# Kernel tuning notes

Measured on AMD Instinct MI355X. Metric: run time of the kernel, lower is better.

Reference implementation:

```python
import jax, jax.numpy as jnp
import numpy as np

N = 100000
E = 1600000

def _gcn_layer(x, row, col, W, b):
    # gather neighbor feats then scatter-add into destination rows
    agg = jax.ops.segment_sum(x[col], row, num_segments=N)  # [N, d]
    deg = jax.ops.segment_sum(jnp.ones((row.shape[0],), x.dtype), row, num_segments=N)
    deg = jnp.clip(deg, 1.0, None)[:, None]  # [N, 1]
    return (agg / deg + x) @ W + b

def setup_inputs() -> dict:
    key = jax.random.key(0)
    ks = jax.random.split(key, 6)
    x = jax.random.normal(ks[0], (N, 64), dtype=jnp.float32)
    edge_index = jax.random.randint(ks[1], (2, E), 0, N, dtype=jnp.int64)
    W1 = jax.random.normal(ks[2], (64, 128), dtype=jnp.float32) * 0.1
    b1 = jax.random.normal(ks[3], (128,), dtype=jnp.float32) * 0.1
    W2 = jax.random.normal(ks[4], (128, 64), dtype=jnp.float32) * 0.1
    b2 = jax.random.normal(ks[5], (64,), dtype=jnp.float32) * 0.1
    return {"x": x, "edge_index": edge_index, "W1": W1, "b1": b1, "W2": W2, "b2": b2}

def reference(x, edge_index, W1, b1, W2, b2):
    row, col = edge_index[0], edge_index[1]
    h = jax.nn.relu(_gcn_layer(x, row, col, W1, b1))
    h = _gcn_layer(h, row, col, W2, b2)
    return h
```

## Files before the change

kernel.cpp:

```cpp
#include <hip/hip_runtime.h>
#include <stdint.h>

#define WS_ALIGN(x) (((x) + 255) & ~(size_t)255)
#define CSR_CAP 64
#define RPB 512
#define CAPB 9216

typedef __attribute__((ext_vector_type(8))) unsigned short ushort8_t;
typedef __attribute__((ext_vector_type(8))) short short8_t;
typedef __attribute__((ext_vector_type(4))) float float4_t;

static __device__ __forceinline__ unsigned short f2bf(float f) {
    unsigned u = __float_as_uint(f);
    unsigned r = (u + 0x7FFFu + ((u >> 16) & 1u)) >> 16;
    return (unsigned short)r;
}
static __device__ __forceinline__ float bf2f(unsigned short s) {
    return __uint_as_float(((unsigned)s) << 16);
}

__global__ void detect_idx_kernel(const int* __restrict__ p, int* __restrict__ flagOr) {
    int t = threadIdx.x;
    int v = 0;
    for (int i = t; i < 2048; i += 256) v |= p[2 * i + 1];
    if (v) atomicOr(flagOr, v);
}

__global__ void init_cursor_kernel(int* __restrict__ gCursor, int nb) {
    int i = blockIdx.x * 256 + threadIdx.x;
    if (i < nb) gCursor[i] = i * CAPB;
}

__global__ __launch_bounds__(256) void bucket_kernel(
    const void* __restrict__ eidx, int E, const int* __restrict__ flagOr,
    int nb, int* __restrict__ gCursor, int2* __restrict__ staging) {
    __shared__ int cnt[256];
    __shared__ int base[256];
    int t = threadIdx.x;
    if (t < nb) cnt[t] = 0;
    __syncthreads();

    int e0 = (blockIdx.x * 256 + t) * 8;
    bool is64 = (*flagOr == 0);
    int m = E - e0; if (m > 8) m = 8; if (m < 0) m = 0;
    int r[8], bk[8], slot[8];
    for (int j = 0; j < m; ++j) {
        r[j] = is64 ? (int)((const long long*)eidx)[e0 + j]
                    : ((const int*)eidx)[e0 + j];
        bk[j] = r[j] >> 9;
        slot[j] = atomicAdd(&cnt[bk[j]], 1);
    }
    __syncthreads();
    if (t < nb) base[t] = atomicAdd(&gCursor[t], cnt[t]);
    __syncthreads();
    for (int j = 0; j < m; ++j) {
        int c = is64 ? (int)((const long long*)eidx)[E + e0 + j]
                     : ((const int*)eidx)[E + e0 + j];
        int dst = base[bk[j]] + slot[j];
        if (dst < (bk[j] + 1) * CAPB) staging[dst] = make_int2(r[j], c);
    }
}

__global__ __launch_bounds__(1024) void ell_kernel(
    const int2* __restrict__ staging, const int* __restrict__ gCursor,
    int* __restrict__ csr, int* __restrict__ deg, int N) {
    __shared__ int lcnt[RPB];
    int b = blockIdx.x, t = threadIdx.x;
    if (t < RPB) lcnt[t] = 0;
    __syncthreads();
    int start = b * CAPB;
    int end = gCursor[b];
    if (end > start + CAPB) end = start + CAPB;
    for (int i = start + t; i < end; i += 1024) {
        int2 rc = staging[i];
        int lr = rc.x - (b << 9);
        int slot = atomicAdd(&lcnt[lr], 1);
        if (slot < CSR_CAP) csr[(size_t)rc.x * CSR_CAP + slot] = rc.y;
    }
    __syncthreads();
    int r = (b << 9) + t;
    if (t < RPB && r < N) deg[r] = lcnt[t];
}

__global__ void xcast_kernel(const float4* __restrict__ x, ushort4* __restrict__ xb,
                             int n4) {
    int i = blockIdx.x * 256 + threadIdx.x;
    if (i >= n4) return;
    float4 f = x[i];
    ushort4 o;
    o.x = f2bf(f.x); o.y = f2bf(f.y); o.z = f2bf(f.z); o.w = f2bf(f.w);
    xb[i] = o;
}

__global__ __launch_bounds__(256) void agg_kernel(
    const unsigned short* __restrict__ xb, const int* __restrict__ deg,
    const int* __restrict__ csr, unsigned short* __restrict__ v, int N) {
    int tid = threadIdx.x;
    int w = tid >> 6, lane = tid & 63;
    int oct = lane >> 3, fo = lane & 7;
    int n = blockIdx.x * 4 + w;
    if (n >= N) return;
    int d = deg[n];
    if (d > CSR_CAP) d = CSR_CAP;
    const int* row = &csr[(size_t)n * CSR_CAP];

    float a0 = 0, a1 = 0, a2 = 0, a3 = 0, a4 = 0, a5 = 0, a6 = 0, a7 = 0;
    int nIter = (d + 7) >> 3;
    int it = 0;
    for (; it + 2 <= nIter; it += 2) {
        int k0 = it * 8 + oct, k1 = k0 + 8;
        int i0 = (k0 < d) ? row[k0] : N;
        int i1 = (k1 < d) ? row[k1] : N;
        ushort8_t f0 = *(const ushort8_t*)&xb[(size_t)i0 * 64 + fo * 8];
        ushort8_t f1 = *(const ushort8_t*)&xb[(size_t)i1 * 64 + fo * 8];
        a0 += bf2f(f0[0]) + bf2f(f1[0]); a1 += bf2f(f0[1]) + bf2f(f1[1]);
        a2 += bf2f(f0[2]) + bf2f(f1[2]); a3 += bf2f(f0[3]) + bf2f(f1[3]);
        a4 += bf2f(f0[4]) + bf2f(f1[4]); a5 += bf2f(f0[5]) + bf2f(f1[5]);
        a6 += bf2f(f0[6]) + bf2f(f1[6]); a7 += bf2f(f0[7]) + bf2f(f1[7]);
    }
    if (it < nIter) {
        int k0 = it * 8 + oct;
        int i0 = (k0 < d) ? row[k0] : N;
        ushort8_t f0 = *(const ushort8_t*)&xb[(size_t)i0 * 64 + fo * 8];
        a0 += bf2f(f0[0]); a1 += bf2f(f0[1]); a2 += bf2f(f0[2]); a3 += bf2f(f0[3]);
        a4 += bf2f(f0[4]); a5 += bf2f(f0[5]); a6 += bf2f(f0[6]); a7 += bf2f(f0[7]);
    }
    #define RED(m) a0 += __shfl_xor(a0, m); a1 += __shfl_xor(a1, m); \
                   a2 += __shfl_xor(a2, m); a3 += __shfl_xor(a3, m); \
                   a4 += __shfl_xor(a4, m); a5 += __shfl_xor(a5, m); \
                   a6 += __shfl_xor(a6, m); a7 += __shfl_xor(a7, m);
    RED(8) RED(16) RED(32)
    #undef RED

    if (oct == 0) {
        ushort8_t s = *(const ushort8_t*)&xb[(size_t)n * 64 + fo * 8];
        float inv = 1.0f / (float)(d > 1 ? d : 1);
        ushort8_t o;
        o[0] = f2bf(a0 * inv + bf2f(s[0])); o[1] = f2bf(a1 * inv + bf2f(s[1]));
        o[2] = f2bf(a2 * inv + bf2f(s[2])); o[3] = f2bf(a3 * inv + bf2f(s[3]));
        o[4] = f2bf(a4 * inv + bf2f(s[4])); o[5] = f2bf(a5 * inv + bf2f(s[5]));
        o[6] = f2bf(a6 * inv + bf2f(s[6])); o[7] = f2bf(a7 * inv + bf2f(s[7]));
        *(ushort8_t*)&v[(size_t)n * 64 + fo * 8] = o;
    }
}

__global__ __launch_bounds__(256) void mlp_kernel(
    const unsigned short* __restrict__ v, const float* __restrict__ W1,
    const float* __restrict__ b1, const float* __restrict__ W2,
    unsigned short* __restrict__ g16, int N) {
    __shared__ unsigned short vA[64 * 72];
    __shared__ unsigned short W1t[128 * 72];
    __shared__ unsigned short hA[64 * 136];
    __shared__ unsigned short W2t[64 * 136];
    int t = threadIdx.x;
    int node0 = blockIdx.x * 64;

    for (int i = t; i < 1024; i += 256) {
        int node = i >> 4, k0 = (i & 15) * 4;
        int gn = node0 + node;
        ushort4 val = make_ushort4(0, 0, 0, 0);
        if (gn < N) val = *(const ushort4*)&v[(size_t)gn * 64 + k0];
        *(ushort4*)&vA[node * 72 + k0] = val;
    }
    for (int i = t; i < 8192; i += 256) {
        int k = i >> 7, col = i & 127;
        W1t[col * 72 + k] = f2bf(W1[i]);
    }
    for (int i = t; i < 8192; i += 256) {
        int k = i >> 6, col = i & 63;
        W2t[col * 136 + k] = f2bf(W2[i]);
    }
    __syncthreads();

    int w = t >> 6, lane = t & 63;
    int l15 = lane & 15, quad = lane >> 4;
    const float4_t fzero = {0.f, 0.f, 0.f, 0.f};

    short8_t af[4][2];
    #pragma unroll
    for (int ms = 0; ms < 4; ++ms)
        #pragma unroll
        for (int kk = 0; kk < 2; ++kk)
            af[ms][kk] = *(const short8_t*)&vA[(ms * 16 + l15) * 72 + kk * 32 + quad * 8];
    short8_t bf1[2][2];
    #pragma unroll
    for (int cs = 0; cs < 2; ++cs)
        #pragma unroll
        for (int kk = 0; kk < 2; ++kk)
            bf1[cs][kk] = *(const short8_t*)&W1t[((w * 2 + cs) * 16 + l15) * 72 + kk * 32 + quad * 8];

    float4_t acc1[4][2];
    #pragma unroll
    for (int ms = 0; ms < 4; ++ms)
        #pragma unroll
        for (int cs = 0; cs < 2; ++cs)
            acc1[ms][cs] = fzero;
    #pragma unroll
    for (int ms = 0; ms < 4; ++ms)
        #pragma unroll
        for (int cs = 0; cs < 2; ++cs) {
            acc1[ms][cs] = __builtin_amdgcn_mfma_f32_16x16x32_bf16(af[ms][0], bf1[cs][0], acc1[ms][cs], 0, 0, 0);
            acc1[ms][cs] = __builtin_amdgcn_mfma_f32_16x16x32_bf16(af[ms][1], bf1[cs][1], acc1[ms][cs], 0, 0, 0);
        }

    #pragma unroll
    for (int cs = 0; cs < 2; ++cs) {
        int col = (w * 2 + cs) * 16 + l15;
        float bias = b1[col];
        #pragma unroll
        for (int ms = 0; ms < 4; ++ms) {
            #pragma unroll
            for (int r = 0; r < 4; ++r) {
                int node = ms * 16 + quad * 4 + r;
                hA[node * 136 + col] = f2bf(fmaxf(acc1[ms][cs][r] + bias, 0.f));
            }
        }
    }
    __syncthreads();

    short8_t bh[4];
    #pragma unroll
    for (int kk = 0; kk < 4; ++kk)
        bh[kk] = *(const short8_t*)&W2t[(w * 16 + l15) * 136 + kk * 32 + quad * 8];

    #pragma unroll
    for (int ms = 0; ms < 4; ++ms) {
        float4_t acc2 = fzero;
        #pragma unroll
        for (int kk = 0; kk < 4; ++kk) {
            short8_t ah = *(const short8_t*)&hA[(ms * 16 + l15) * 136 + kk * 32 + quad * 8];
            acc2 = __builtin_amdgcn_mfma_f32_16x16x32_bf16(ah, bh[kk], acc2, 0, 0, 0);
        }
        #pragma unroll
        for (int r = 0; r < 4; ++r) {
            int gn = node0 + ms * 16 + quad * 4 + r;
            if (gn < N) g16[(size_t)gn * 64 + w * 16 + l15] = f2bf(acc2[r]);
        }
    }
}

__global__ __launch_bounds__(256) void final_kernel(
    const unsigned short* __restrict__ g16, const float* __restrict__ b2,
    const int* __restrict__ deg, const int* __restrict__ csr,
    float* __restrict__ out, int N) {
    int tid = threadIdx.x;
    int w = tid >> 6, lane = tid & 63;
    int oct = lane >> 3, fo = lane & 7;
    int n = blockIdx.x * 4 + w;
    if (n >= N) return;
    int d = deg[n];
    if (d > CSR_CAP) d = CSR_CAP;
    const int* row = &csr[(size_t)n * CSR_CAP];

    float a0 = 0, a1 = 0, a2 = 0, a3 = 0, a4 = 0, a5 = 0, a6 = 0, a7 = 0;
    int nIter = (d + 7) >> 3;
    int it = 0;
    for (; it + 2 <= nIter; it += 2) {
        int k0 = it * 8 + oct, k1 = k0 + 8;
        int i0 = (k0 < d) ? row[k0] : N;
        int i1 = (k1 < d) ? row[k1] : N;
        ushort8_t f0 = *(const ushort8_t*)&g16[(size_t)i0 * 64 + fo * 8];
        ushort8_t f1 = *(const ushort8_t*)&g16[(size_t)i1 * 64 + fo * 8];
        a0 += bf2f(f0[0]) + bf2f(f1[0]); a1 += bf2f(f0[1]) + bf2f(f1[1]);
        a2 += bf2f(f0[2]) + bf2f(f1[2]); a3 += bf2f(f0[3]) + bf2f(f1[3]);
        a4 += bf2f(f0[4]) + bf2f(f1[4]); a5 += bf2f(f0[5]) + bf2f(f1[5]);
        a6 += bf2f(f0[6]) + bf2f(f1[6]); a7 += bf2f(f0[7]) + bf2f(f1[7]);
    }
    if (it < nIter) {
        int k0 = it * 8 + oct;
        int i0 = (k0 < d) ? row[k0] : N;
        ushort8_t f0 = *(const ushort8_t*)&g16[(size_t)i0 * 64 + fo * 8];
        a0 += bf2f(f0[0]); a1 += bf2f(f0[1]); a2 += bf2f(f0[2]); a3 += bf2f(f0[3]);
        a4 += bf2f(f0[4]); a5 += bf2f(f0[5]); a6 += bf2f(f0[6]); a7 += bf2f(f0[7]);
    }
    #define RED(m) a0 += __shfl_xor(a0, m); a1 += __shfl_xor(a1, m); \
                   a2 += __shfl_xor(a2, m); a3 += __shfl_xor(a3, m); \
                   a4 += __shfl_xor(a4, m); a5 += __shfl_xor(a5, m); \
                   a6 += __shfl_xor(a6, m); a7 += __shfl_xor(a7, m);
    RED(8) RED(16) RED(32)
    #undef RED

    if (oct == 0) {
        ushort8_t s = *(const ushort8_t*)&g16[(size_t)n * 64 + fo * 8];
        float4 bzA = ((const float4*)b2)[fo * 2];
        float4 bzB = ((const float4*)b2)[fo * 2 + 1];
        float inv = 1.0f / (float)(d > 1 ? d : 1);
        float4 oA, oB;
        oA.x = a0 * inv + bf2f(s[0]) + bzA.x;
        oA.y = a1 * inv + bf2f(s[1]) + bzA.y;
        oA.z = a2 * inv + bf2f(s[2]) + bzA.z;
        oA.w = a3 * inv + bf2f(s[3]) + bzA.w;
        oB.x = a4 * inv + bf2f(s[4]) + bzB.x;
        oB.y = a5 * inv + bf2f(s[5]) + bzB.y;
        oB.z = a6 * inv + bf2f(s[6]) + bzB.z;
        oB.w = a7 * inv + bf2f(s[7]) + bzB.w;
        *(float4*)&out[(size_t)n * 64 + fo * 8] = oA;
        *(float4*)&out[(size_t)n * 64 + fo * 8 + 4] = oB;
    }
}

extern "C" void kernel_launch(void* const* d_in, const int* in_sizes, int n_in,
                              void* d_out, int out_size, void* d_ws, size_t ws_size,
                              hipStream_t stream) {
    const float* x  = (const float*)d_in[0];
    const void*  ei = d_in[1];
    const float* W1 = (const float*)d_in[2];
    const float* b1 = (const float*)d_in[3];
    const float* W2 = (const float*)d_in[4];
    const float* b2 = (const float*)d_in[5];
    float* out = (float*)d_out;

    int N = out_size / 64;
    int E = in_sizes[1] / 2;
    int nb = (N + RPB - 1) / RPB;

    char* ws = (char*)d_ws;
    size_t off = 0;
    auto alloc = [&](size_t bytes) { size_t r = off; off += WS_ALIGN(bytes); return r; };
    int* flagOr  = (int*)(ws + alloc(4));
    int* gCursor = (int*)(ws + alloc((size_t)4 * nb));
    int* deg     = (int*)(ws + alloc((size_t)4 * N));
    int* csr     = (int*)(ws + alloc((size_t)4 * N * CSR_CAP));
    char* bufA   = ws + alloc((size_t)128 * (N + 1));
    unsigned short* xb  = (unsigned short*)bufA;
    unsigned short* g16 = (unsigned short*)bufA;
    unsigned short* v   = (unsigned short*)(ws + alloc((size_t)128 * N));
    int2* staging = (int2*)(ws + alloc((size_t)8 * nb * CAPB));
    (void)ws_size;

    hipMemsetAsync(flagOr, 0, 4, stream);
    hipMemsetAsync(bufA + (size_t)128 * N, 0, 128, stream);

    detect_idx_kernel<<<1, 256, 0, stream>>>((const int*)ei, flagOr);
    init_cursor_kernel<<<(nb + 255) / 256, 256, 0, stream>>>(gCursor, nb);

    int b1blocks = (E + 2047) / 2048;
    bucket_kernel<<<b1blocks, 256, 0, stream>>>(ei, E, flagOr, nb, gCursor, staging);
    ell_kernel<<<nb, 1024, 0, stream>>>(staging, gCursor, csr, deg, N);

    xcast_kernel<<<(N * 16 + 255) / 256, 256, 0, stream>>>((const float4*)x, (ushort4*)xb, N * 16);
    agg_kernel<<<(N + 3) / 4, 256, 0, stream>>>(xb, deg, csr, v, N);
    mlp_kernel<<<(N + 63) / 64, 256, 0, stream>>>(v, W1, b1, W2, g16, N);
    final_kernel<<<(N + 3) / 4, 256, 0, stream>>>(g16, b2, deg, csr, out, N);
}
```

Measured before the change: 250.6 us.

## Fuse prep kernels, fuse aggregation into MLP, pack staging entries, change gather mapping

Merges the bf16 cast, index-width detection, cursor init, sentinel zeroing and one-time weight transposition into a single prep kernel, so weights are no longer transposed in every MLP block. Fuses the first-layer aggregation into the MLP kernel so aggregated rows go straight to shared memory instead of a global buffer. Packs staging entries into 32-bit words (local row plus column), which halves bucket traffic. Remaps the gather so each half-wave handles one node with 4-byte loads over 4 neighbours at a time, with no shuffle reduction. Risks: the packing limits column indices to 17 bits, and the fused kernel has less parallelism per block during the gather phase.

```diff
diff --git a/kernel.cpp b/kernel.cpp
--- a/kernel.cpp
+++ b/kernel.cpp
@@ -6,7 +6,6 @@
 #define RPB 512
 #define CAPB 9216
 
-typedef __attribute__((ext_vector_type(8))) unsigned short ushort8_t;
 typedef __attribute__((ext_vector_type(8))) short short8_t;
 typedef __attribute__((ext_vector_type(4))) float float4_t;
 
@@ -19,21 +18,48 @@
     return __uint_as_float(((unsigned)s) << 16);
 }
 
-__global__ void detect_idx_kernel(const int* __restrict__ p, int* __restrict__ flagOr) {
-    int t = threadIdx.x;
-    int v = 0;
-    for (int i = t; i < 2048; i += 256) v |= p[2 * i + 1];
-    if (v) atomicOr(flagOr, v);
-}
-
-__global__ void init_cursor_kernel(int* __restrict__ gCursor, int nb) {
-    int i = blockIdx.x * 256 + threadIdx.x;
-    if (i < nb) gCursor[i] = i * CAPB;
+__global__ __launch_bounds__(256) void prep_kernel(
+    const float4* __restrict__ x, ushort4* __restrict__ xb, int n4,
+    const int* __restrict__ eip, int* __restrict__ flagOr,
+    const float* __restrict__ W1, unsigned short* __restrict__ W1t,
+    const float* __restrict__ W2, unsigned short* __restrict__ W2t,
+    int* __restrict__ gCursor, int nb,
+    unsigned short* __restrict__ sentX, unsigned short* __restrict__ sentG) {
+    int gt = blockIdx.x * 256 + threadIdx.x;
+    if (gt < n4) {
+        float4 f = x[gt];
+        ushort4 o;
+        o.x = f2bf(f.x); o.y = f2bf(f.y); o.z = f2bf(f.z); o.w = f2bf(f.w);
+        xb[gt] = o;
+        return;
+    }
+    int r = gt - n4;
+    if (r < 8192) {
+        int k = r >> 7, col = r & 127;
+        W1t[col * 64 + k] = f2bf(W1[r]);
+        return;
+    }
+    r -= 8192;
+    if (r < 8192) {
+        int k = r >> 6, col = r & 63;
+        W2t[col * 128 + k] = f2bf(W2[r]);
+        return;
+    }
+    r -= 8192;
+    if (r < 256) { if (r < nb) gCursor[r] = r * CAPB; return; }
+    r -= 256;
+    if (r < 64) { sentX[r] = 0; sentG[r] = 0; return; }
+    r -= 64;
+    if (r < 256) {
+        int v = 0;
+        for (int i = r; i < 2048; i += 256) v |= eip[2 * i + 1];
+        if (v) atomicOr(flagOr, v);
+    }
 }
 
 __global__ __launch_bounds__(256) void bucket_kernel(
     const void* __restrict__ eidx, int E, const int* __restrict__ flagOr,
-    int nb, int* __restrict__ gCursor, int2* __restrict__ staging) {
+    int nb, int* __restrict__ gCursor, unsigned* __restrict__ staging) {
     __shared__ int cnt[256];
     __shared__ int base[256];
     int t = threadIdx.x;
@@ -57,12 +83,13 @@
         int c = is64 ? (int)((const long long*)eidx)[E + e0 + j]
                      : ((const int*)eidx)[E + e0 + j];
         int dst = base[bk[j]] + slot[j];
-        if (dst < (bk[j] + 1) * CAPB) staging[dst] = make_int2(r[j], c);
+        if (dst < (bk[j] + 1) * CAPB)
+            staging[dst] = ((unsigned)(r[j] & (RPB - 1)) << 17) | (unsigned)c;
     }
 }
 
 __global__ __launch_bounds__(1024) void ell_kernel(
-    const int2* __restrict__ staging, const int* __restrict__ gCursor,
+    const unsigned* __restrict__ staging, const int* __restrict__ gCursor,
     int* __restrict__ csr, int* __restrict__ deg, int N) {
     __shared__ int lcnt[RPB];
     int b = blockIdx.x, t = threadIdx.x;
@@ -72,122 +99,75 @@
     int end = gCursor[b];
     if (end > start + CAPB) end = start + CAPB;
     for (int i = start + t; i < end; i += 1024) {
-        int2 rc = staging[i];
-        int lr = rc.x - (b << 9);
+        unsigned u = staging[i];
+        int lr = (int)(u >> 17);
+        int c  = (int)(u & 0x1FFFF);
         int slot = atomicAdd(&lcnt[lr], 1);
-        if (slot < CSR_CAP) csr[(size_t)rc.x * CSR_CAP + slot] = rc.y;
-    }
-    __syncthreads();
-    int r = (b << 9) + t;
-    if (t < RPB && r < N) deg[r] = lcnt[t];
-}
-
-__global__ void xcast_kernel(const float4* __restrict__ x, ushort4* __restrict__ xb,
-                             int n4) {
-    int i = blockIdx.x * 256 + threadIdx.x;
-    if (i >= n4) return;
-    float4 f = x[i];
-    ushort4 o;
-    o.x = f2bf(f.x); o.y = f2bf(f.y); o.z = f2bf(f.z); o.w = f2bf(f.w);
-    xb[i] = o;
-}
-
-__global__ __launch_bounds__(256) void agg_kernel(
+        if (slot < CSR_CAP) csr[(size_t)((b << 9) + lr) * CSR_CAP + slot] = c;
+    }
+    __syncthreads();
+    int rr = (b << 9) + t;
+    if (t < RPB && rr < N) deg[rr] = lcnt[t];
+}
+
+__global__ __launch_bounds__(256) void agg_mlp_kernel(
     const unsigned short* __restrict__ xb, const int* __restrict__ deg,
-    const int* __restrict__ csr, unsigned short* __restrict__ v, int N) {
-    int tid = threadIdx.x;
-    int w = tid >> 6, lane = tid & 63;
-    int oct = lane >> 3, fo = lane & 7;
-    int n = blockIdx.x * 4 + w;
-    if (n >= N) return;
-    int d = deg[n];
-    if (d > CSR_CAP) d = CSR_CAP;
-    const int* row = &csr[(size_t)n * CSR_CAP];
-
-    float a0 = 0, a1 = 0, a2 = 0, a3 = 0, a4 = 0, a5 = 0, a6 = 0, a7 = 0;
-    int nIter = (d + 7) >> 3;
-    int it = 0;
-    for (; it + 2 <= nIter; it += 2) {
-        int k0 = it * 8 + oct, k1 = k0 + 8;
-        int i0 = (k0 < d) ? row[k0] : N;
-        int i1 = (k1 < d) ? row[k1] : N;
-        ushort8_t f0 = *(const ushort8_t*)&xb[(size_t)i0 * 64 + fo * 8];
-        ushort8_t f1 = *(const ushort8_t*)&xb[(size_t)i1 * 64 + fo * 8];
-        a0 += bf2f(f0[0]) + bf2f(f1[0]); a1 += bf2f(f0[1]) + bf2f(f1[1]);
-        a2 += bf2f(f0[2]) + bf2f(f1[2]); a3 += bf2f(f0[3]) + bf2f(f1[3]);
-        a4 += bf2f(f0[4]) + bf2f(f1[4]); a5 += bf2f(f0[5]) + bf2f(f1[5]);
-        a6 += bf2f(f0[6]) + bf2f(f1[6]); a7 += bf2f(f0[7]) + bf2f(f1[7]);
-    }
-    if (it < nIter) {
-        int k0 = it * 8 + oct;
-        int i0 = (k0 < d) ? row[k0] : N;
-        ushort8_t f0 = *(const ushort8_t*)&xb[(size_t)i0 * 64 + fo * 8];
-        a0 += bf2f(f0[0]); a1 += bf2f(f0[1]); a2 += bf2f(f0[2]); a3 += bf2f(f0[3]);
-        a4 += bf2f(f0[4]); a5 += bf2f(f0[5]); a6 += bf2f(f0[6]); a7 += bf2f(f0[7]);
-    }
-    #define RED(m) a0 += __shfl_xor(a0, m); a1 += __shfl_xor(a1, m); \
-                   a2 += __shfl_xor(a2, m); a3 += __shfl_xor(a3, m); \
-                   a4 += __shfl_xor(a4, m); a5 += __shfl_xor(a5, m); \
-                   a6 += __shfl_xor(a6, m); a7 += __shfl_xor(a7, m);
-    RED(8) RED(16) RED(32)
-    #undef RED
-
-    if (oct == 0) {
-        ushort8_t s = *(const ushort8_t*)&xb[(size_t)n * 64 + fo * 8];
-        float inv = 1.0f / (float)(d > 1 ? d : 1);
-        ushort8_t o;
-        o[0] = f2bf(a0 * inv + bf2f(s[0])); o[1] = f2bf(a1 * inv + bf2f(s[1]));
-        o[2] = f2bf(a2 * inv + bf2f(s[2])); o[3] = f2bf(a3 * inv + bf2f(s[3]));
-        o[4] = f2bf(a4 * inv + bf2f(s[4])); o[5] = f2bf(a5 * inv + bf2f(s[5]));
-        o[6] = f2bf(a6 * inv + bf2f(s[6])); o[7] = f2bf(a7 * inv + bf2f(s[7]));
-        *(ushort8_t*)&v[(size_t)n * 64 + fo * 8] = o;
-    }
-}
-
-__global__ __launch_bounds__(256) void mlp_kernel(
-    const unsigned short* __restrict__ v, const float* __restrict__ W1,
-    const float* __restrict__ b1, const float* __restrict__ W2,
+    const int* __restrict__ csr, const unsigned short* __restrict__ W1t,
+    const float* __restrict__ b1, const unsigned short* __restrict__ W2t,
     unsigned short* __restrict__ g16, int N) {
     __shared__ unsigned short vA[64 * 72];
-    __shared__ unsigned short W1t[128 * 72];
     __shared__ unsigned short hA[64 * 136];
-    __shared__ unsigned short W2t[64 * 136];
     int t = threadIdx.x;
     int node0 = blockIdx.x * 64;
-
-    for (int i = t; i < 1024; i += 256) {
-        int node = i >> 4, k0 = (i & 15) * 4;
-        int gn = node0 + node;
-        ushort4 val = make_ushort4(0, 0, 0, 0);
-        if (gn < N) val = *(const ushort4*)&v[(size_t)gn * 64 + k0];
-        *(ushort4*)&vA[node * 72 + k0] = val;
-    }
-    for (int i = t; i < 8192; i += 256) {
-        int k = i >> 7, col = i & 127;
-        W1t[col * 72 + k] = f2bf(W1[i]);
-    }
-    for (int i = t; i < 8192; i += 256) {
-        int k = i >> 6, col = i & 63;
-        W2t[col * 136 + k] = f2bf(W2[i]);
-    }
-    __syncthreads();
-
-    int w = t >> 6, lane = t & 63;
+    int wv = t >> 6, lane = t & 63;
+    int h = lane >> 5, fl = lane & 31;
+
+    for (int pass = 0; pass < 8; ++pass) {
+        int ln = wv * 16 + pass * 2 + h;
+        int n = node0 + ln;
+        bool valid = (n < N);
+        int nn = valid ? n : N;
+        int d = valid ? deg[n] : 0;
+        if (d > CSR_CAP) d = CSR_CAP;
+        const int* row = &csr[(size_t)nn * CSR_CAP];
+        int dOther = __shfl_xor(d, 32);
+        int dmax = d > dOther ? d : dOther;
+        float ax0 = 0, ay0 = 0, ax1 = 0, ay1 = 0;
+        float ax2 = 0, ay2 = 0, ax3 = 0, ay3 = 0;
+        for (int k = 0; k < dmax; k += 4) {
+            int i0 = (k     < d) ? row[k]     : N;
+            int i1 = (k + 1 < d) ? row[k + 1] : N;
+            int i2 = (k + 2 < d) ? row[k + 2] : N;
+            int i3 = (k + 3 < d) ? row[k + 3] : N;
+            ushort2 u0 = *(const ushort2*)&xb[(size_t)i0 * 64 + 2 * fl];
+            ushort2 u1 = *(const ushort2*)&xb[(size_t)i1 * 64 + 2 * fl];
+            ushort2 u2 = *(const ushort2*)&xb[(size_t)i2 * 64 + 2 * fl];
+            ushort2 u3 = *(const ushort2*)&xb[(size_t)i3 * 64 + 2 * fl];
+            ax0 += bf2f(u0.x); ay0 += bf2f(u0.y);
+            ax1 += bf2f(u1.x); ay1 += bf2f(u1.y);
+            ax2 += bf2f(u2.x); ay2 += bf2f(u2.y);
+            ax3 += bf2f(u3.x); ay3 += bf2f(u3.y);
+        }
+        float ax = (ax0 + ax1) + (ax2 + ax3);
+        float ay = (ay0 + ay1) + (ay2 + ay3);
+        ushort2 s = *(const ushort2*)&xb[(size_t)nn * 64 + 2 * fl];
+        float inv = 1.0f / (float)(d > 1 ? d : 1);
+        ushort2 o;
+        o.x = f2bf(ax * inv + bf2f(s.x));
+        o.y = f2bf(ay * inv + bf2f(s.y));
+        *(ushort2*)&vA[ln * 72 + 2 * fl] = o;
+    }
+    __syncthreads();
+
     int l15 = lane & 15, quad = lane >> 4;
     const float4_t fzero = {0.f, 0.f, 0.f, 0.f};
 
-    short8_t af[4][2];
-    #pragma unroll
-    for (int ms = 0; ms < 4; ++ms)
+    short8_t bf1[2][2];
+    #pragma unroll
+    for (int cs = 0; cs < 2; ++cs)
         #pragma unroll
         for (int kk = 0; kk < 2; ++kk)
-            af[ms][kk] = *(const short8_t*)&vA[(ms * 16 + l15) * 72 + kk * 32 + quad * 8];
-    short8_t bf1[2][2];
-    #pragma unroll
-    for (int cs = 0; cs < 2; ++cs)
-        #pragma unroll
-        for (int kk = 0; kk < 2; ++kk)
-            bf1[cs][kk] = *(const short8_t*)&W1t[((w * 2 + cs) * 16 + l15) * 72 + kk * 32 + quad * 8];
+            bf1[cs][kk] = *(const short8_t*)&W1t[(size_t)((wv * 2 + cs) * 16 + l15) * 64 + kk * 32 + quad * 8];
 
     float4_t acc1[4][2];
     #pragma unroll
@@ -196,32 +176,34 @@
         for (int cs = 0; cs < 2; ++cs)
             acc1[ms][cs] = fzero;
     #pragma unroll
-    for (int ms = 0; ms < 4; ++ms)
+    for (int ms = 0; ms < 4; ++ms) {
+        short8_t af0 = *(const short8_t*)&vA[(ms * 16 + l15) * 72 + quad * 8];
+        short8_t af1 = *(const short8_t*)&vA[(ms * 16 + l15) * 72 + 32 + quad * 8];
         #pragma unroll
         for (int cs = 0; cs < 2; ++cs) {
-            acc1[ms][cs] = __builtin_amdgcn_mfma_f32_16x16x32_bf16(af[ms][0], bf1[cs][0], acc1[ms][cs], 0, 0, 0);
-            acc1[ms][cs] = __builtin_amdgcn_mfma_f32_16x16x32_bf16(af[ms][1], bf1[cs][1], acc1[ms][cs], 0, 0, 0);
+            acc1[ms][cs] = __builtin_amdgcn_mfma_f32_16x16x32_bf16(af0, bf1[cs][0], acc1[ms][cs], 0, 0, 0);
+            acc1[ms][cs] = __builtin_amdgcn_mfma_f32_16x16x32_bf16(af1, bf1[cs][1], acc1[ms][cs], 0, 0, 0);
         }
+    }
 
     #pragma unroll
     for (int cs = 0; cs < 2; ++cs) {
-        int col = (w * 2 + cs) * 16 + l15;
+        int col = (wv * 2 + cs) * 16 + l15;
         float bias = b1[col];
         #pragma unroll
-        for (int ms = 0; ms < 4; ++ms) {
+        for (int ms = 0; ms < 4; ++ms)
             #pragma unroll
             for (int r = 0; r < 4; ++r) {
                 int node = ms * 16 + quad * 4 + r;
                 hA[node * 136 + col] = f2bf(fmaxf(acc1[ms][cs][r] + bias, 0.f));
             }
-        }
     }
     __syncthreads();
 
     short8_t bh[4];
     #pragma unroll
     for (int kk = 0; kk < 4; ++kk)
-        bh[kk] = *(const short8_t*)&W2t[(w * 16 + l15) * 136 + kk * 32 + quad * 8];
+        bh[kk] = *(const short8_t*)&W2t[(size_t)(wv * 16 + l15) * 128 + kk * 32 + quad * 8];
 
     #pragma unroll
     for (int ms = 0; ms < 4; ++ms) {
@@ -234,7 +216,7 @@
         #pragma unroll
         for (int r = 0; r < 4; ++r) {
             int gn = node0 + ms * 16 + quad * 4 + r;
-            if (gn < N) g16[(size_t)gn * 64 + w * 16 + l15] = f2bf(acc2[r]);
+            if (gn < N) g16[(size_t)gn * 64 + wv * 16 + l15] = f2bf(acc2[r]);
         }
     }
 }
@@ -243,59 +225,43 @@
     const unsigned short* __restrict__ g16, const float* __restrict__ b2,
     const int* __restrict__ deg, const int* __restrict__ csr,
     float* __restrict__ out, int N) {
-    int tid = threadIdx.x;
-    int w = tid >> 6, lane = tid & 63;
-    int oct = lane >> 3, fo = lane & 7;
-    int n = blockIdx.x * 4 + w;
-    if (n >= N) return;
-    int d = deg[n];
+    int t = threadIdx.x;
+    int wv = t >> 6, lane = t & 63;
+    int h = lane >> 5, fl = lane & 31;
+    int n = blockIdx.x * 8 + wv * 2 + h;
+    bool valid = (n < N);
+    int nn = valid ? n : N;
+    int d = valid ? deg[n] : 0;
     if (d > CSR_CAP) d = CSR_CAP;
-    const int* row = &csr[(size_t)n * CSR_CAP];
-
-    float a0 = 0, a1 = 0, a2 = 0, a3 = 0, a4 = 0, a5 = 0, a6 = 0, a7 = 0;
-    int nIter = (d + 7) >> 3;
-    int it = 0;
-    for (; it + 2 <= nIter; it += 2) {
-        int k0 = it * 8 + oct, k1 = k0 + 8;
-        int i0 = (k0 < d) ? row[k0] : N;
-        int i1 = (k1 < d) ? row[k1] : N;
-        ushort8_t f0 = *(const ushort8_t*)&g16[(size_t)i0 * 64 + fo * 8];
-        ushort8_t f1 = *(const ushort8_t*)&g16[(size_t)i1 * 64 + fo * 8];
-        a0 += bf2f(f0[0]) + bf2f(f1[0]); a1 += bf2f(f0[1]) + bf2f(f1[1]);
-        a2 += bf2f(f0[2]) + bf2f(f1[2]); a3 += bf2f(f0[3]) + bf2f(f1[3]);
-        a4 += bf2f(f0[4]) + bf2f(f1[4]); a5 += bf2f(f0[5]) + bf2f(f1[5]);
-        a6 += bf2f(f0[6]) + bf2f(f1[6]); a7 += bf2f(f0[7]) + bf2f(f1[7]);
-    }
-    if (it < nIter) {
-        int k0 = it * 8 + oct;
-        int i0 = (k0 < d) ? row[k0] : N;
-        ushort8_t f0 = *(const ushort8_t*)&g16[(size_t)i0 * 64 + fo * 8];
-        a0 += bf2f(f0[0]); a1 += bf2f(f0[1]); a2 += bf2f(f0[2]); a3 += bf2f(f0[3]);
-        a4 += bf2f(f0[4]); a5 += bf2f(f0[5]); a6 += bf2f(f0[6]); a7 += bf2f(f0[7]);
-    }
-    #define RED(m) a0 += __shfl_xor(a0, m); a1 += __shfl_xor(a1, m); \
-                   a2 += __shfl_xor(a2, m); a3 += __shfl_xor(a3, m); \
-                   a4 += __shfl_xor(a4, m); a5 += __shfl_xor(a5, m); \
-                   a6 += __shfl_xor(a6, m); a7 += __shfl_xor(a7, m);
-    RED(8) RED(16) RED(32)
-    #undef RED
-
-    if (oct == 0) {
-        ushort8_t s = *(const ushort8_t*)&g16[(size_t)n * 64 + fo * 8];
-        float4 bzA = ((const float4*)b2)[fo * 2];
-        float4 bzB = ((const float4*)b2)[fo * 2 + 1];
+    const int* row = &csr[(size_t)nn * CSR_CAP];
+    int dOther = __shfl_xor(d, 32);
+    int dmax = d > dOther ? d : dOther;
+    float ax0 = 0, ay0 = 0, ax1 = 0, ay1 = 0;
+    float ax2 = 0, ay2 = 0, ax3 = 0, ay3 = 0;
+    for (int k = 0; k < dmax; k += 4) {
+        int i0 = (k     < d) ? row[k]     : N;
+        int i1 = (k + 1 < d) ? row[k + 1] : N;
+        int i2 = (k + 2 < d) ? row[k + 2] : N;
+        int i3 = (k + 3 < d) ? row[k + 3] : N;
+        ushort2 u0 = *(const ushort2*)&g16[(size_t)i0 * 64 + 2 * fl];
+        ushort2 u1 = *(const ushort2*)&g16[(size_t)i1 * 64 + 2 * fl];
+        ushort2 u2 = *(const ushort2*)&g16[(size_t)i2 * 64 + 2 * fl];
+        ushort2 u3 = *(const ushort2*)&g16[(size_t)i3 * 64 + 2 * fl];
+        ax0 += bf2f(u0.x); ay0 += bf2f(u0.y);
+        ax1 += bf2f(u1.x); ay1 += bf2f(u1.y);
+        ax2 += bf2f(u2.x); ay2 += bf2f(u2.y);
+        ax3 += bf2f(u3.x); ay3 += bf2f(u3.y);
+    }
+    if (valid) {
+        float ax = (ax0 + ax1) + (ax2 + ax3);
+        float ay = (ay0 + ay1) + (ay2 + ay3);
+        ushort2 s = *(const ushort2*)&g16[(size_t)n * 64 + 2 * fl];
+        float2 bz = ((const float2*)b2)[fl];
         float inv = 1.0f / (float)(d > 1 ? d : 1);
-        float4 oA, oB;
-        oA.x = a0 * inv + bf2f(s[0]) + bzA.x;
-        oA.y = a1 * inv + bf2f(s[1]) + bzA.y;
-        oA.z = a2 * inv + bf2f(s[2]) + bzA.z;
-        oA.w = a3 * inv + bf2f(s[3]) + bzA.w;
-        oB.x = a4 * inv + bf2f(s[4]) + bzB.x;
-        oB.y = a5 * inv + bf2f(s[5]) + bzB.y;
-        oB.z = a6 * inv + bf2f(s[6]) + bzB.z;
-        oB.w = a7 * inv + bf2f(s[7]) + bzB.w;
-        *(float4*)&out[(size_t)n * 64 + fo * 8] = oA;
-        *(float4*)&out[(size_t)n * 64 + fo * 8 + 4] = oB;
+        float2 o;
+        o.x = ax * inv + bf2f(s.x) + bz.x;
+        o.y = ay * inv + bf2f(s.y) + bz.y;
+        *(float2*)&out[(size_t)n * 64 + 2 * fl] = o;
     }
 }
 
@@ -321,25 +287,25 @@
     int* gCursor = (int*)(ws + alloc((size_t)4 * nb));
     int* deg     = (int*)(ws + alloc((size_t)4 * N));
     int* csr     = (int*)(ws + alloc((size_t)4 * N * CSR_CAP));
-    char* bufA   = ws + alloc((size_t)128 * (N + 1));
-    unsigned short* xb  = (unsigned short*)bufA;
-    unsigned short* g16 = (unsigned short*)bufA;
-    unsigned short* v   = (unsigned short*)(ws + alloc((size_t)128 * N));
-    int2* staging = (int2*)(ws + alloc((size_t)8 * nb * CAPB));
+    unsigned short* xb  = (unsigned short*)(ws + alloc((size_t)128 * (N + 1)));
+    unsigned short* g16 = (unsigned short*)(ws + alloc((size_t)128 * (N + 1)));
+    unsigned short* W1t = (unsigned short*)(ws + alloc((size_t)2 * 8192));
+    unsigned short* W2t = (unsigned short*)(ws + alloc((size_t)2 * 8192));
+    unsigned* staging   = (unsigned*)(ws + alloc((size_t)4 * nb * CAPB));
     (void)ws_size;
 
     hipMemsetAsync(flagOr, 0, 4, stream);
-    hipMemsetAsync(bufA + (size_t)128 * N, 0, 128, stream);
-
-    detect_idx_kernel<<<1, 256, 0, stream>>>((const int*)ei, flagOr);
-    init_cursor_kernel<<<(nb + 255) / 256, 256, 0, stream>>>(gCursor, nb);
-
-    int b1blocks = (E + 2047) / 2048;
-    bucket_kernel<<<b1blocks, 256, 0, stream>>>(ei, E, flagOr, nb, gCursor, staging);
+
+    int n4 = N * 16;
+    int prepThreads = n4 + 8192 + 8192 + 256 + 64 + 256;
+    prep_kernel<<<(prepThreads + 255) / 256, 256, 0, stream>>>(
+        (const float4*)x, (ushort4*)xb, n4, (const int*)ei, flagOr,
+        W1, W1t, W2, W2t, gCursor, nb, &xb[(size_t)N * 64], &g16[(size_t)N * 64]);
+
+    int bblocks = (E + 2047) / 2048;
+    bucket_kernel<<<bblocks, 256, 0, stream>>>(ei, E, flagOr, nb, gCursor, staging);
     ell_kernel<<<nb, 1024, 0, stream>>>(staging, gCursor, csr, deg, N);
 
-    xcast_kernel<<<(N * 16 + 255) / 256, 256, 0, stream>>>((const float4*)x, (ushort4*)xb, N * 16);
-    agg_kernel<<<(N + 3) / 4, 256, 0, stream>>>(xb, deg, csr, v, N);
-    mlp_kernel<<<(N + 63) / 64, 256, 0, stream>>>(v, W1, b1, W2, g16, N);
-    final_kernel<<<(N + 3) / 4, 256, 0, stream>>>(g16, b2, deg, csr, out, N);
-}
+    agg_mlp_kernel<<<(N + 63) / 64, 256, 0, stream>>>(xb, deg, csr, W1t, b1, W2t, g16, N);
+    final_kernel<<<(N + 7) / 8, 256, 0, stream>>>(g16, b2, deg, csr, out, N);
+}
```

After: 254.5 us. Within noise of the previous version (+1.6%).
